# Performance work log

Measured on AMD Instinct MI355X. Metric: run time of the kernel, lower is better.

The kernel has to match this reference:

```python
import jax, jax.numpy as jnp
import numpy as np
from jax import lax


def _viterbi_decode(logits, trans):
    """Batched Viterbi decode (tf.contrib.crf.crf_decode semantics, full lengths).
    logits: [B, T, U] unary potentials; trans: [U, U], trans[i, j] = score(i -> j).
    Returns int32 tags [B, T]."""
    logits_t = jnp.swapaxes(logits, 0, 1)  # [T, B, U]
    init_v = logits_t[0]                   # [B, U]

    def fwd_step(v, logit_t):
        # scores[b, i, j] = v[b, i] + trans[i, j]
        scores = v[:, :, None] + trans[None, :, :]          # [B, U, U]
        bp = jnp.argmax(scores, axis=1).astype(jnp.int32)   # [B, U] best prev tag
        v_new = jnp.max(scores, axis=1) + logit_t           # [B, U]
        return v_new, bp

    v_last, bps = lax.scan(fwd_step, init_v, logits_t[1:])  # bps: [T-1, B, U]
    last_tag = jnp.argmax(v_last, axis=1).astype(jnp.int32)  # [B]

    def bwd_step(tag, bp):
        # tag is the tag at t+1; bp[b, k] = best tag at t given tag k at t+1
        new_tag = jnp.take_along_axis(bp, tag[:, None], axis=1)[:, 0]
        return new_tag, new_tag

    _, tags_prefix = lax.scan(bwd_step, last_tag, bps, reverse=True)  # [T-1, B]
    tags = jnp.concatenate([tags_prefix, last_tag[None, :]], axis=0)  # [T, B]
    return jnp.swapaxes(tags, 0, 1)  # [B, T]


def setup_inputs() -> dict:
    key = jax.random.key(0)
    k0, k1, k2, k3, k4 = jax.random.split(key, 5)
    B, T, D, U = 64, 512, 1024, 128
    x = jax.random.normal(k0, (B, T, D), dtype=jnp.float32)
    kernel = jax.random.normal(k1, (D, U), dtype=jnp.float32) * (1.0 / np.sqrt(D))
    bias = jnp.zeros((U,), dtype=jnp.float32)
    chain_kernel = jax.random.normal(k2, (U, U), dtype=jnp.float32) * 0.1
    left_boundary = jax.random.normal(k3, (U,), dtype=jnp.float32) * 0.1
    right_boundary = jax.random.normal(k4, (U,), dtype=jnp.float32) * 0.1
    return {
        "x": x,
        "kernel": kernel,
        "bias": bias,
        "chain_kernel": chain_kernel,
        "left_boundary": left_boundary,
        "right_boundary": right_boundary,
    }


def reference(x, kernel, bias, chain_kernel, left_boundary, right_boundary):
    # _dense_layer: linear activation, x @ kernel + bias
    logits = jnp.einsum("btd,du->btu", x, kernel) + bias  # [B, T, U]
    # add_boundary_energy with mask=None: boundaries on first / last timestep
    logits = logits.at[:, 0, :].add(left_boundary)
    logits = logits.at[:, -1, :].add(right_boundary)
    # test_mode='viterbi', learn_mode='join': return decoded tags cast to float32
    tags = _viterbi_decode(logits, chain_kernel)
    return tags.astype(jnp.float32)
```

## Files before the change

kernel.cpp:

```cpp
#include <hip/hip_runtime.h>

#define T_SEQ 512
#define U_TAGS 128
#define D_DIM 1024

__global__ __launch_bounds__(256) void crf_gemm(
    const float* __restrict__ A, const float* __restrict__ Bk,
    const float* __restrict__ bias, const float* __restrict__ lb,
    const float* __restrict__ rb, float* __restrict__ C) {
  __shared__ float As[16][132];
  __shared__ float Bs[16][132];
  const int tid = threadIdx.x;
  const int tx = tid & 15, ty = tid >> 4;
  const int row0 = blockIdx.x * 128;

  const int am = tid >> 2, ak = (tid & 3) << 2;
  const int bk = tid >> 5, bn = (tid & 31) << 2;

  float acc[8][8] = {};

  float4 a0 = *(const float4*)&A[(size_t)(row0 + am) * D_DIM + ak];
  float4 a1 = *(const float4*)&A[(size_t)(row0 + am + 64) * D_DIM + ak];
  float4 b0 = *(const float4*)&Bk[(size_t)bk * U_TAGS + bn];
  float4 b1 = *(const float4*)&Bk[(size_t)(bk + 8) * U_TAGS + bn];

  for (int k0 = 0; k0 < D_DIM; k0 += 16) {
    As[ak + 0][am] = a0.x; As[ak + 1][am] = a0.y;
    As[ak + 2][am] = a0.z; As[ak + 3][am] = a0.w;
    As[ak + 0][am + 64] = a1.x; As[ak + 1][am + 64] = a1.y;
    As[ak + 2][am + 64] = a1.z; As[ak + 3][am + 64] = a1.w;
    *(float4*)&Bs[bk][bn] = b0;
    *(float4*)&Bs[bk + 8][bn] = b1;
    __syncthreads();
    if (k0 + 16 < D_DIM) {
      a0 = *(const float4*)&A[(size_t)(row0 + am) * D_DIM + k0 + 16 + ak];
      a1 = *(const float4*)&A[(size_t)(row0 + am + 64) * D_DIM + k0 + 16 + ak];
      b0 = *(const float4*)&Bk[(size_t)(k0 + 16 + bk) * U_TAGS + bn];
      b1 = *(const float4*)&Bk[(size_t)(k0 + 16 + bk + 8) * U_TAGS + bn];
    }
#pragma unroll
    for (int kk = 0; kk < 16; ++kk) {
      float a[8], b[8];
      *(float4*)&a[0] = *(const float4*)&As[kk][ty * 8];
      *(float4*)&a[4] = *(const float4*)&As[kk][ty * 8 + 4];
      *(float4*)&b[0] = *(const float4*)&Bs[kk][tx * 4];
      *(float4*)&b[4] = *(const float4*)&Bs[kk][tx * 4 + 64];
#pragma unroll
      for (int r = 0; r < 8; ++r)
#pragma unroll
        for (int c = 0; c < 8; ++c) acc[r][c] = fmaf(a[r], b[c], acc[r][c]);
    }
    __syncthreads();
  }

#pragma unroll
  for (int r = 0; r < 8; ++r) {
    const int row = row0 + ty * 8 + r;
    const int t = row & (T_SEQ - 1);
    const int n0 = tx * 4, n1 = tx * 4 + 64;
    float o[8];
#pragma unroll
    for (int c = 0; c < 4; ++c) {
      float v = acc[r][c] + bias[n0 + c];
      if (t == 0) v += lb[n0 + c];
      if (t == T_SEQ - 1) v += rb[n0 + c];
      o[c] = v;
    }
#pragma unroll
    for (int c = 0; c < 4; ++c) {
      float v = acc[r][c + 4] + bias[n1 + c];
      if (t == 0) v += lb[n1 + c];
      if (t == T_SEQ - 1) v += rb[n1 + c];
      o[c + 4] = v;
    }
    *(float4*)&C[(size_t)row * U_TAGS + n0] = *(float4*)&o[0];
    *(float4*)&C[(size_t)row * U_TAGS + n1] = *(float4*)&o[4];
  }
}

__device__ __forceinline__ void barrier_lds_only() {
  asm volatile("s_waitcnt lgkmcnt(0)\n\ts_barrier" ::: "memory");
}
__device__ __forceinline__ float fmax_dpp1(float m) {
  int i = __builtin_amdgcn_mov_dpp(__float_as_int(m), 0xB1, 0xF, 0xF, true);
  return fmaxf(m, __int_as_float(i));
}
__device__ __forceinline__ float fmax_dpp2(float m) {
  int i = __builtin_amdgcn_mov_dpp(__float_as_int(m), 0x4E, 0xF, 0xF, true);
  return fmaxf(m, __int_as_float(i));
}
__device__ __forceinline__ int imin_dpp1(int v) {
  int i = __builtin_amdgcn_mov_dpp(v, 0xB1, 0xF, 0xF, true);
  return v < i ? v : i;
}
__device__ __forceinline__ int imin_dpp2(int v) {
  int i = __builtin_amdgcn_mov_dpp(v, 0x4E, 0xF, 0xF, true);
  return v < i ? v : i;
}
__device__ __forceinline__ float max3f(float a, float b, float c) {
  return fmaxf(fmaxf(a, b), c);
}

__global__ __launch_bounds__(512) void crf_viterbi(
    const float* __restrict__ logits,
    const float* __restrict__ trans,
    float* __restrict__ out) {
  __shared__ __align__(16) float vbuf[2][4][136];
  __shared__ __align__(16) unsigned char bp[T_SEQ * U_TAGS];
  __shared__ unsigned char tags[T_SEQ];
  __shared__ unsigned char M[8][U_TAGS];
  __shared__ int seedL[8];
  __shared__ float red_v[8];
  __shared__ int red_i[8];

  const int b = blockIdx.x;
  const int tid = threadIdx.x;
  const int j = tid >> 2;
  const int seg = tid & 3;
  const float* lg_b = logits + (size_t)b * T_SEQ * U_TAGS;

  float* tstage = (float*)bp;
#pragma unroll
  for (int it = 0; it < 8; ++it)
    *(float4*)&tstage[(it * 512 + tid) * 4] =
        *(const float4*)&trans[(it * 512 + tid) * 4];
  __syncthreads();
  float tr[32];
#pragma unroll
  for (int e = 0; e < 32; ++e) tr[e] = tstage[(seg * 32 + e) * U_TAGS + j];
  if (tid < U_TAGS) {
    float v0 = lg_b[tid];
#pragma unroll
    for (int cp = 0; cp < 4; ++cp) vbuf[0][cp][tid] = v0;
  }
  __syncthreads();

  float lgp0 = lg_b[1 * U_TAGS + j];
  float lgp1 = lg_b[2 * U_TAGS + j];
  for (int t = 1; t < T_SEQ; ++t) {
    int tp = t + 2; if (tp > T_SEQ - 1) tp = T_SEQ - 1;
    float lgnew = lg_b[(size_t)tp * U_TAGS + j];

    const float* vrow = &vbuf[(t - 1) & 1][seg][seg * 32];
    float s[32];
#pragma unroll
    for (int q = 0; q < 8; ++q) {
      float4 vv = *(const float4*)&vrow[q * 4];
      s[q * 4 + 0] = vv.x + tr[q * 4 + 0];
      s[q * 4 + 1] = vv.y + tr[q * 4 + 1];
      s[q * 4 + 2] = vv.z + tr[q * 4 + 2];
      s[q * 4 + 3] = vv.w + tr[q * 4 + 3];
    }
    float a0 = max3f(s[0], s[1], s[2]),   a1 = max3f(s[3], s[4], s[5]);
    float a2 = max3f(s[6], s[7], s[8]),   a3 = max3f(s[9], s[10], s[11]);
    float a4 = max3f(s[12], s[13], s[14]), a5 = max3f(s[15], s[16], s[17]);
    float a6 = max3f(s[18], s[19], s[20]), a7 = max3f(s[21], s[22], s[23]);
    float a8 = max3f(s[24], s[25], s[26]), a9 = max3f(s[27], s[28], s[29]);
    float a10 = fmaxf(s[30], s[31]);
    float b0 = max3f(a0, a1, a2), b1 = max3f(a3, a4, a5);
    float b2 = max3f(a6, a7, a8), b3 = fmaxf(a9, a10);
    float m = fmaxf(max3f(b0, b1, b2), b3);
    m = fmax_dpp1(m);
    m = fmax_dpp2(m);
    int e0 = 127, e1 = 127, e2 = 127, e3 = 127;
#pragma unroll
    for (int e = 7; e >= 0; --e) {
      e0 = (s[e] == m) ? e : e0;
      e1 = (s[8 + e] == m) ? 8 + e : e1;
      e2 = (s[16 + e] == m) ? 16 + e : e2;
      e3 = (s[24 + e] == m) ? 24 + e : e3;
    }
    int el = min(min(e0, e1), min(e2, e3));
    int ic = (el < 127) ? seg * 32 + el : 1023;
    ic = imin_dpp1(ic);
    ic = imin_dpp2(ic);
    if (seg == 0) {
      float vn = m + lgp0;
#pragma unroll
      for (int cp = 0; cp < 4; ++cp) vbuf[t & 1][cp][j] = vn;
      bp[(t - 1) * U_TAGS + j] = (unsigned char)ic;
    }
    lgp0 = lgp1;
    lgp1 = lgnew;
    barrier_lds_only();
  }

  if (tid < U_TAGS) {
    float val = vbuf[1][0][tid];
    int idx = tid;
#pragma unroll
    for (int off = 1; off < 64; off <<= 1) {
      float vo = __shfl_xor(val, off);
      int io = __shfl_xor(idx, off);
      if (vo > val || (vo == val && io < idx)) { val = vo; idx = io; }
    }
    if ((tid & 63) == 0) { red_v[tid >> 6] = val; red_i[tid >> 6] = idx; }
  }
  __syncthreads();
  if (tid == 0) {
    int tg = (red_v[1] > red_v[0]) ? red_i[1] : red_i[0];
    tags[T_SEQ - 1] = (unsigned char)tg;
  }
  __syncthreads();

  const int w = tid >> 6, l = tid & 63;
  const int lo = w * 64;
  const int hi = (w == 7) ? (T_SEQ - 2) : (w * 64 + 63);
  {
    int c0 = l, c1 = l + 64;
    for (int t = hi; t >= lo; --t) {
      c0 = bp[t * U_TAGS + c0];
      c1 = bp[t * U_TAGS + c1];
    }
    M[w][l] = (unsigned char)c0;
    M[w][l + 64] = (unsigned char)c1;
  }
  __syncthreads();
  if (tid == 0) {
    int sd = tags[T_SEQ - 1];
    seedL[7] = sd;
    for (int w2 = 7; w2 >= 1; --w2) { sd = M[w2][sd]; seedL[w2 - 1] = sd; }
  }
  __syncthreads();
  if (l == 0) {
    int cur = seedL[w];
    for (int t = hi; t >= lo; --t) {
      cur = bp[t * U_TAGS + cur];
      tags[t] = (unsigned char)cur;
    }
  }
  __syncthreads();
  out[(size_t)b * T_SEQ + tid] = (float)tags[tid];
}

extern "C" void kernel_launch(void* const* d_in, const int* in_sizes, int n_in,
                              void* d_out, int out_size, void* d_ws,
                              size_t ws_size, hipStream_t stream) {
  const float* x = (const float*)d_in[0];
  const float* kern = (const float*)d_in[1];
  const float* bias = (const float*)d_in[2];
  const float* chain = (const float*)d_in[3];
  const float* lb = (const float*)d_in[4];
  const float* rb = (const float*)d_in[5];
  float* out = (float*)d_out;
  float* logits = (float*)d_ws;

  crf_gemm<<<256, 256, 0, stream>>>(x, kern, bias, lb, rb, logits);
  crf_viterbi<<<64, 512, 0, stream>>>(logits, chain, out);
}
```

Measured before the change: 602.3 us.

## Split GEMM reduction dimension in two to double block count

Adds a split-K variant of the logits GEMM that launches 512 blocks, each covering half of D, and writes partial sums to two workspace buffers. A separate combine kernel adds the partials plus bias and boundary energies. The aim is better CU occupancy, since 256 blocks underfill the MI355X. The cost is an extra kernel launch and roughly 32 MB of additional partial-sum traffic. The new path only runs when the workspace is large enough, and otherwise falls back to the original GEMM.

```diff
diff --git a/kernel.cpp b/kernel.cpp
--- a/kernel.cpp
+++ b/kernel.cpp
@@ -3,6 +3,91 @@
 #define T_SEQ 512
 #define U_TAGS 128
 #define D_DIM 1024
+#define M_ROWS (64 * T_SEQ)
+
+__global__ __launch_bounds__(256) void crf_gemm_half(
+    const float* __restrict__ A, const float* __restrict__ Bk,
+    float* __restrict__ Cpart) {
+  __shared__ float As[16][132];
+  __shared__ float Bs[16][132];
+  const int tid = threadIdx.x;
+  const int tx = tid & 15, ty = tid >> 4;
+  const int row0 = blockIdx.x * 128;
+  const int kbase = blockIdx.y * (D_DIM / 2);
+
+  const int am = tid >> 2, ak = (tid & 3) << 2;
+  const int bk = tid >> 5, bn = (tid & 31) << 2;
+
+  float acc[8][8] = {};
+
+  float4 a0 = *(const float4*)&A[(size_t)(row0 + am) * D_DIM + kbase + ak];
+  float4 a1 = *(const float4*)&A[(size_t)(row0 + am + 64) * D_DIM + kbase + ak];
+  float4 b0 = *(const float4*)&Bk[(size_t)(kbase + bk) * U_TAGS + bn];
+  float4 b1 = *(const float4*)&Bk[(size_t)(kbase + bk + 8) * U_TAGS + bn];
+
+  for (int k0 = 0; k0 < D_DIM / 2; k0 += 16) {
+    As[ak + 0][am] = a0.x; As[ak + 1][am] = a0.y;
+    As[ak + 2][am] = a0.z; As[ak + 3][am] = a0.w;
+    As[ak + 0][am + 64] = a1.x; As[ak + 1][am + 64] = a1.y;
+    As[ak + 2][am + 64] = a1.z; As[ak + 3][am + 64] = a1.w;
+    *(float4*)&Bs[bk][bn] = b0;
+    *(float4*)&Bs[bk + 8][bn] = b1;
+    __syncthreads();
+    if (k0 + 16 < D_DIM / 2) {
+      const int kn = kbase + k0 + 16;
+      a0 = *(const float4*)&A[(size_t)(row0 + am) * D_DIM + kn + ak];
+      a1 = *(const float4*)&A[(size_t)(row0 + am + 64) * D_DIM + kn + ak];
+      b0 = *(const float4*)&Bk[(size_t)(kn + bk) * U_TAGS + bn];
+      b1 = *(const float4*)&Bk[(size_t)(kn + bk + 8) * U_TAGS + bn];
+    }
+#pragma unroll
+    for (int kk = 0; kk < 16; ++kk) {
+      float a[8], b[8];
+      *(float4*)&a[0] = *(const float4*)&As[kk][ty * 8];
+      *(float4*)&a[4] = *(const float4*)&As[kk][ty * 8 + 4];
+      *(float4*)&b[0] = *(const float4*)&Bs[kk][tx * 4];
+      *(float4*)&b[4] = *(const float4*)&Bs[kk][tx * 4 + 64];
+#pragma unroll
+      for (int r = 0; r < 8; ++r)
+#pragma unroll
+        for (int c = 0; c < 8; ++c) acc[r][c] = fmaf(a[r], b[c], acc[r][c]);
+    }
+    __syncthreads();
+  }
+
+  float* Cp = Cpart + (size_t)blockIdx.y * M_ROWS * U_TAGS;
+#pragma unroll
+  for (int r = 0; r < 8; ++r) {
+    const int row = row0 + ty * 8 + r;
+    *(float4*)&Cp[(size_t)row * U_TAGS + tx * 4] = *(float4*)&acc[r][0];
+    *(float4*)&Cp[(size_t)row * U_TAGS + tx * 4 + 64] = *(float4*)&acc[r][4];
+  }
+}
+
+__global__ __launch_bounds__(256) void crf_combine(
+    float* __restrict__ p, const float* __restrict__ bias,
+    const float* __restrict__ lb, const float* __restrict__ rb) {
+  const int i = blockIdx.x * 256 + threadIdx.x;
+  const int row = i >> 5;
+  const int col = (i & 31) << 2;
+  const int t = row & (T_SEQ - 1);
+  const float* p1 = p + (size_t)M_ROWS * U_TAGS;
+  float4 v0 = *(const float4*)&p[(size_t)i * 4];
+  float4 v1 = *(const float4*)&p1[(size_t)i * 4];
+  float4 bb = *(const float4*)&bias[col];
+  float4 o;
+  o.x = v0.x + v1.x + bb.x; o.y = v0.y + v1.y + bb.y;
+  o.z = v0.z + v1.z + bb.z; o.w = v0.w + v1.w + bb.w;
+  if (t == 0) {
+    float4 l = *(const float4*)&lb[col];
+    o.x += l.x; o.y += l.y; o.z += l.z; o.w += l.w;
+  }
+  if (t == T_SEQ - 1) {
+    float4 r = *(const float4*)&rb[col];
+    o.x += r.x; o.y += r.y; o.z += r.z; o.w += r.w;
+  }
+  *(float4*)&p[(size_t)i * 4] = o;
+}
 
 __global__ __launch_bounds__(256) void crf_gemm(
     const float* __restrict__ A, const float* __restrict__ Bk,
@@ -13,17 +98,13 @@
   const int tid = threadIdx.x;
   const int tx = tid & 15, ty = tid >> 4;
   const int row0 = blockIdx.x * 128;
-
   const int am = tid >> 2, ak = (tid & 3) << 2;
   const int bk = tid >> 5, bn = (tid & 31) << 2;
-
   float acc[8][8] = {};
-
   float4 a0 = *(const float4*)&A[(size_t)(row0 + am) * D_DIM + ak];
   float4 a1 = *(const float4*)&A[(size_t)(row0 + am + 64) * D_DIM + ak];
   float4 b0 = *(const float4*)&Bk[(size_t)bk * U_TAGS + bn];
   float4 b1 = *(const float4*)&Bk[(size_t)(bk + 8) * U_TAGS + bn];
-
   for (int k0 = 0; k0 < D_DIM; k0 += 16) {
     As[ak + 0][am] = a0.x; As[ak + 1][am] = a0.y;
     As[ak + 2][am] = a0.z; As[ak + 3][am] = a0.w;
@@ -52,7 +133,6 @@
     }
     __syncthreads();
   }
-
 #pragma unroll
   for (int r = 0; r < 8; ++r) {
     const int row = row0 + ty * 8 + r;
@@ -245,6 +325,13 @@
   float* out = (float*)d_out;
   float* logits = (float*)d_ws;
 
-  crf_gemm<<<256, 256, 0, stream>>>(x, kern, bias, lb, rb, logits);
+  const size_t part = (size_t)M_ROWS * U_TAGS * sizeof(float);
+  if (ws_size >= 2 * part) {
+    crf_gemm_half<<<dim3(256, 2), 256, 0, stream>>>(x, kern, logits);
+    crf_combine<<<(M_ROWS * U_TAGS / 4 + 255) / 256, 256, 0, stream>>>(
+        logits, bias, lb, rb);
+  } else {
+    crf_gemm<<<256, 256, 0, stream>>>(x, kern, bias, lb, rb, logits);
+  }
   crf_viterbi<<<64, 512, 0, stream>>>(logits, chain, out);
 }
```

Measured after the change: 591.4 us. No clear change (-1.8%).
